# Performance work log

Hardware: AMD Instinct MI355X
Metric: run time of the kernel (lower is better)

The kernel has to match this reference:

```python
import jax, jax.numpy as jnp
import numpy as np

VOCAB = 32000; DIM = 512; NL = 6; B = 2; L = 1024
DI = 2 * DIM      # d_inner (expand=2)
DS = 16           # d_state
DC = 4            # d_conv
DR = DIM // 16    # dt_rank = ceil(512/16) = 32


def setup_inputs() -> dict:
    key = jax.random.key(0)
    ks = jax.random.split(key, 10)
    s = 0.02
    tokens = jax.random.randint(ks[0], (B, L), 0, VOCAB)
    pos_emb = jax.random.normal(ks[1], (1, L, DIM)) * s
    embed = jax.random.normal(ks[2], (VOCAB, DIM)) * s
    lm_w = jax.random.normal(ks[3], (VOCAB, DIM)) * s
    lm_b = jnp.zeros((VOCAB,), jnp.float32)
    in_proj_w = jax.random.normal(ks[4], (NL, 2 * DI, DIM)) * s
    conv_w = jax.random.normal(ks[5], (NL, DI, DC)) * s
    conv_b = jnp.zeros((NL, DI), jnp.float32)
    x_proj_w = jax.random.normal(ks[6], (NL, DR + 2 * DS, DI)) * s
    dt_proj_w = jax.random.normal(ks[7], (NL, DI, DR)) * s
    dt_proj_b = jnp.broadcast_to(jnp.log(jnp.expm1(jnp.float32(0.01))), (NL, DI)).astype(jnp.float32)
    A_log = jnp.log(jnp.broadcast_to(jnp.arange(1, DS + 1, dtype=jnp.float32), (NL, DI, DS)))
    Dp = jnp.ones((NL, DI), jnp.float32)
    out_w = jax.random.normal(ks[8], (NL, DIM, DI)) * s
    ln_g = jnp.ones((NL, DIM), jnp.float32)
    ln_b = jnp.zeros((NL, DIM), jnp.float32)
    return dict(tokens=tokens, pos_emb=pos_emb, embed=embed, lm_w=lm_w, lm_b=lm_b,
                in_proj_w=in_proj_w, conv_w=conv_w, conv_b=conv_b, x_proj_w=x_proj_w,
                dt_proj_w=dt_proj_w, dt_proj_b=dt_proj_b, A_log=A_log, Dp=Dp,
                out_w=out_w, ln_g=ln_g, ln_b=ln_b)


def silu(x):
    return x * jax.nn.sigmoid(x)


def layernorm(x, g, b, eps=1e-5):
    mu = jnp.mean(x, -1, keepdims=True)
    var = jnp.var(x, -1, keepdims=True)
    return (x - mu) * jax.lax.rsqrt(var + eps) * g + b


def causal_dwconv(x, w, b):
    # x: (B,L,DI), w: (DI,DC) depthwise, left-pad causal
    xp = jnp.pad(x, ((0, 0), (DC - 1, 0), (0, 0)))
    y = b
    for k in range(DC):
        y = y + w[:, k] * xp[:, k:k + x.shape[1], :]
    return y


def selective_scan(u, dt, A, Bm, Cm, Dp):
    # u,dt: (B,L,DI); A: (DI,DS); Bm,Cm: (B,L,DS)
    dA = jnp.exp(dt[..., None] * A)                       # (B,L,DI,DS)
    dBu = dt[..., None] * Bm[:, :, None, :] * u[..., None]
    h0 = jnp.zeros((u.shape[0], DI, DS), u.dtype)

    def step(h, inp):
        dA_t, dBu_t, C_t = inp
        h = dA_t * h + dBu_t
        y = jnp.einsum('bdn,bn->bd', h, C_t)
        return h, y

    _, ys = jax.lax.scan(step, h0, (dA.transpose(1, 0, 2, 3),
                                    dBu.transpose(1, 0, 2, 3),
                                    Cm.transpose(1, 0, 2)))
    return ys.transpose(1, 0, 2) + u * Dp


def mamba_block(x, in_w, cw, cb, xp_w, dtw, dtb, A_log, Dp, ow):
    xz = jnp.einsum('bld,ed->ble', x, in_w)               # (B,L,2*DI)
    xc, z = jnp.split(xz, 2, axis=-1)
    xc = silu(causal_dwconv(xc, cw, cb))
    x_dbl = jnp.einsum('bld,ed->ble', xc, xp_w)           # (B,L,DR+2*DS)
    dt, Bm, Cm = jnp.split(x_dbl, [DR, DR + DS], axis=-1)
    dt = jax.nn.softplus(jnp.einsum('blr,dr->bld', dt, dtw) + dtb)
    A = -jnp.exp(A_log)
    y = selective_scan(xc, dt, A, Bm, Cm, Dp)
    y = y * silu(z)
    return jnp.einsum('bld,ed->ble', y, ow)


def reference(tokens, pos_emb, embed, lm_w, lm_b, in_proj_w, conv_w, conv_b,
              x_proj_w, dt_proj_w, dt_proj_b, A_log, Dp, out_w, ln_g, ln_b):
    x = embed[tokens] + pos_emb[:, :tokens.shape[1]]
    for i in range(NL):
        res = x
        x = mamba_block(x, in_proj_w[i], conv_w[i], conv_b[i], x_proj_w[i],
                        dt_proj_w[i], dt_proj_b[i], A_log[i], Dp[i], out_w[i])
        x = layernorm(x + res, ln_g[i], ln_b[i])
    return jnp.einsum('bld,vd->blv', x, lm_w) + lm_b
```

## Files before the change

### kernel.cpp

```cpp
#include <hip/hip_runtime.h>
#include <hip/hip_bf16.h>
#include <math.h>

#define BB 2
#define LL 1024
#define DIM 512
#define NL 6
#define DI 1024
#define DS 16
#define DC 4
#define DR 32
#define VOCAB 32000
#define M_ROWS (BB * LL)
#define CCH 64
#define CHLEN (LL / CCH)
#define KSPLIT 8
#define OSPLIT 2

typedef unsigned short u16;
typedef __attribute__((ext_vector_type(8))) short bf16x8;
typedef __attribute__((ext_vector_type(4))) float f32x4;

__device__ __forceinline__ u16 f2bf(float f) {
    unsigned u = __float_as_uint(f);
    u += 0x7FFF + ((u >> 16) & 1);
    return (u16)(u >> 16);
}
__device__ __forceinline__ float bf2f(u16 h) {
    return __uint_as_float(((unsigned)h) << 16);
}
#define SWZ(r, c) ((c) ^ (((r) >> 1) & 3))

__global__ __launch_bounds__(256) void cast_all(const float* __restrict__ lm,
                                                const float* __restrict__ inw,
                                                const float* __restrict__ ow,
                                                const float* __restrict__ xp,
                                                u16* __restrict__ lmb,
                                                u16* __restrict__ inb,
                                                u16* __restrict__ owb_,
                                                u16* __restrict__ xpb) {
    int idx = blockIdx.x * 256 + threadIdx.x;
    const float* src; u16* dst; int off;
    if (idx < 2048000)      { src = lm;  dst = lmb;  off = idx; }
    else if (idx < 2834432) { src = inw; dst = inb;  off = idx - 2048000; }
    else if (idx < 3227648) { src = ow;  dst = owb_; off = idx - 2834432; }
    else                    { src = xp;  dst = xpb;  off = idx - 3227648; }
    float4 v0 = ((const float4*)src)[off * 2];
    float4 v1 = ((const float4*)src)[off * 2 + 1];
    union { u16 h[8]; int4 v; } r;
    r.h[0] = f2bf(v0.x); r.h[1] = f2bf(v0.y); r.h[2] = f2bf(v0.z); r.h[3] = f2bf(v0.w);
    r.h[4] = f2bf(v1.x); r.h[5] = f2bf(v1.y); r.h[6] = f2bf(v1.z); r.h[7] = f2bf(v1.w);
    ((int4*)dst)[off] = r.v;
}

__global__ __launch_bounds__(256) void embed_kernel(const int* __restrict__ tok,
                                                    const float* __restrict__ pos,
                                                    const float* __restrict__ emb,
                                                    float* __restrict__ x,
                                                    u16* __restrict__ xb) {
    int idx = blockIdx.x * 256 + threadIdx.x;
    int d = idx & (DIM - 1);
    int l = (idx >> 9) & (LL - 1);
    int b = idx >> 19;
    int t = tok[b * LL + l];
    float v = emb[(size_t)t * DIM + d] + pos[l * DIM + d];
    x[idx] = v;
    xb[idx] = f2bf(v);
}

__global__ __launch_bounds__(512) void gemm_256(const u16* __restrict__ A,
                                                const u16* __restrict__ W,
                                                float* __restrict__ C,
                                                const float* __restrict__ bias,
                                                int K, int N) {
    __shared__ __align__(16) char smem_raw[98304];
    u16* As = (u16*)smem_raw;
    u16* Ws = (u16*)(smem_raw + 49152);
    float* Cs = (float*)smem_raw;

    const int t = threadIdx.x;
    const int l = t & 63;
    const int w = t >> 6;
    const int wr = w >> 2;
    const int wc = w & 3;

    const int nwg = gridDim.x;
    const int q8 = nwg >> 3, r8 = nwg & 7;
    const int xcd = blockIdx.x & 7, rank = blockIdx.x >> 3;
    const int wgid = (xcd < r8 ? xcd * (q8 + 1) : r8 * (q8 + 1) + (xcd - r8) * q8) + rank;
    const int bm = (wgid & 7) * 256;
    const int bn = (wgid >> 3) * 256;

    f32x4 acc[8][4] = {};
    const int nt = K >> 5;

    auto STAGE = [&](int bufi, int k0) {
#pragma unroll
        for (int p = 0; p < 2; ++p) {
            const int g = p * 512 + t;
            const int row = g >> 2, slot = g & 3;
            __builtin_amdgcn_global_load_lds(
                (const __attribute__((address_space(1))) unsigned int*)
                    (A + (size_t)(bm + row) * K + k0 + SWZ(row, slot) * 8),
                (__attribute__((address_space(3))) unsigned int*)
                    (As + bufi * 8192 + (p * 512 + w * 64) * 8),
                16, 0, 0);
        }
#pragma unroll
        for (int p = 0; p < 2; ++p) {
            const int g = p * 512 + t;
            const int row = g >> 2, slot = g & 3;
            __builtin_amdgcn_global_load_lds(
                (const __attribute__((address_space(1))) unsigned int*)
                    (W + (size_t)(bn + row) * K + k0 + SWZ(row, slot) * 8),
                (__attribute__((address_space(3))) unsigned int*)
                    (Ws + bufi * 8192 + (p * 512 + w * 64) * 8),
                16, 0, 0);
        }
    };
    auto COMPUTE = [&](int bufi) {
        const u16* Ab = As + bufi * 8192;
        const u16* Wb = Ws + bufi * 8192;
        bf16x8 bfr[4];
#pragma unroll
        for (int ni = 0; ni < 4; ++ni) {
            const int wrow = wc * 64 + ni * 16 + (l & 15);
            bfr[ni] = *(const bf16x8*)(Wb + wrow * 32 + SWZ(wrow, l >> 4) * 8);
        }
#pragma unroll
        for (int mi = 0; mi < 8; ++mi) {
            const int arow = wr * 128 + mi * 16 + (l & 15);
            bf16x8 a = *(const bf16x8*)(Ab + arow * 32 + SWZ(arow, l >> 4) * 8);
#pragma unroll
            for (int ni = 0; ni < 4; ++ni)
                acc[mi][ni] = __builtin_amdgcn_mfma_f32_16x16x32_bf16(bfr[ni], a, acc[mi][ni], 0, 0, 0);
        }
    };

    STAGE(0, 0);
    STAGE(1, 32);
    int b0 = 0;
    for (int tt = 0; tt < nt - 2; ++tt) {
        int b2 = b0 + 2; if (b2 >= 3) b2 -= 3;
        STAGE(b2, (tt + 2) << 5);
        asm volatile("s_waitcnt vmcnt(8)\ns_barrier" ::: "memory");
        COMPUTE(b0);
        asm volatile("s_waitcnt lgkmcnt(0)\ns_barrier" ::: "memory");
        ++b0; if (b0 == 3) b0 = 0;
    }
    asm volatile("s_waitcnt vmcnt(4)\ns_barrier" ::: "memory");
    COMPUTE(b0);
    asm volatile("s_waitcnt lgkmcnt(0)\ns_barrier" ::: "memory");
    ++b0; if (b0 == 3) b0 = 0;
    asm volatile("s_waitcnt vmcnt(0)\ns_barrier" ::: "memory");
    COMPUTE(b0);
    asm volatile("s_waitcnt lgkmcnt(0)" ::: "memory");
    __syncthreads();

#pragma unroll
    for (int pass = 0; pass < 4; ++pass) {
        if (wr == (pass >> 1)) {
            const int pm0 = (pass & 1) * 4;
#pragma unroll
            for (int mi2 = 0; mi2 < 4; ++mi2) {
                const int r = mi2 * 16 + (l & 15);
#pragma unroll
                for (int ni = 0; ni < 4; ++ni) {
                    const int c = wc * 64 + ni * 16 + ((l >> 4) << 2);
                    float4 v;
                    v.x = acc[pm0 + mi2][ni][0]; v.y = acc[pm0 + mi2][ni][1];
                    v.z = acc[pm0 + mi2][ni][2]; v.w = acc[pm0 + mi2][ni][3];
                    *(float4*)(Cs + r * 260 + c) = v;
                }
            }
        }
        __syncthreads();
#pragma unroll
        for (int it = 0; it < 8; ++it) {
            const int idx = it * 512 + t;
            const int r = idx >> 6;
            const int c4 = (idx & 63) * 4;
            float4 v = *(float4*)(Cs + r * 260 + c4);
            if (bias != nullptr) {
                float4 b4 = *(const float4*)(bias + bn + c4);
                v.x += b4.x; v.y += b4.y; v.z += b4.z; v.w += b4.w;
            }
            *(float4*)(C + (size_t)(bm + pass * 64 + r) * N + bn + c4) = v;
        }
        __syncthreads();
    }
}

__global__ __launch_bounds__(256) void gemm_n64(const u16* __restrict__ A,
                                                const u16* __restrict__ W,
                                                float* __restrict__ out,
                                                u16* __restrict__ outb,
                                                const float* __restrict__ bias,
                                                int lda, int ldw, int ldc,
                                                int KS, int pstride) {
    __shared__ __align__(16) char smem_raw[36864];
    u16* As = (u16*)smem_raw;
    u16* Ws = (u16*)(smem_raw + 24576);
    float* Cs = (float*)smem_raw;

    const int t = threadIdx.x;
    const int l = t & 63;
    const int w = t >> 6;
    const int gx = gridDim.x, gy = gridDim.y;
    const int nwg = gx * gy * gridDim.z;
    const int fid = (blockIdx.z * gy + blockIdx.y) * gx + blockIdx.x;
    const int q8 = nwg >> 3, r8 = nwg & 7;
    const int xcd = fid & 7, rank = fid >> 3;
    const int wgid = (xcd < r8 ? xcd * (q8 + 1) : r8 * (q8 + 1) + (xcd - r8) * q8) + rank;
    const int kz = wgid % gx;
    const int bm = ((wgid / gx) % gy) * 128;
    const int bnn = (wgid / (gx * gy)) * 64;
    const int wm = w * 32;

    f32x4 acc[2][4] = {};
    const int nt = KS >> 5;
    const int kbeg = kz * KS;

    auto STAGE = [&](int bufi, int k0) {
#pragma unroll
        for (int p = 0; p < 2; ++p) {
            const int i = p * 256 + w * 64 + l;
            const int row = i >> 2;
            const int kq = SWZ(row, i & 3);
            __builtin_amdgcn_global_load_lds(
                (const __attribute__((address_space(1))) unsigned int*)
                    (A + (size_t)(bm + row) * lda + k0 + kq * 8),
                (__attribute__((address_space(3))) unsigned int*)
                    (As + bufi * 4096 + (p * 256 + w * 64) * 8),
                16, 0, 0);
        }
        {
            const int i = w * 64 + l;
            const int row = i >> 2;
            const int kq = SWZ(row, i & 3);
            __builtin_amdgcn_global_load_lds(
                (const __attribute__((address_space(1))) unsigned int*)
                    (W + (size_t)(bnn + row) * ldw + k0 + kq * 8),
                (__attribute__((address_space(3))) unsigned int*)
                    (Ws + bufi * 2048 + (w * 64) * 8),
                16, 0, 0);
        }
    };
    auto COMPUTE = [&](int bufi) {
        const u16* Ab = As + bufi * 4096;
        const u16* Wb = Ws + bufi * 2048;
        bf16x8 bfr[4];
#pragma unroll
        for (int ni = 0; ni < 4; ++ni) {
            const int wr2 = ni * 16 + (l & 15);
            bfr[ni] = *(const bf16x8*)(Wb + wr2 * 32 + SWZ(wr2, l >> 4) * 8);
        }
#pragma unroll
        for (int mi = 0; mi < 2; ++mi) {
            const int ar = wm + mi * 16 + (l & 15);
            bf16x8 a = *(const bf16x8*)(Ab + ar * 32 + SWZ(ar, l >> 4) * 8);
#pragma unroll
            for (int ni = 0; ni < 4; ++ni)
                acc[mi][ni] = __builtin_amdgcn_mfma_f32_16x16x32_bf16(bfr[ni], a, acc[mi][ni], 0, 0, 0);
        }
    };

    STAGE(0, kbeg);
    if (nt == 1) {
        asm volatile("s_waitcnt vmcnt(0)\ns_barrier" ::: "memory");
        COMPUTE(0);
        asm volatile("s_waitcnt lgkmcnt(0)" ::: "memory");
    } else {
        STAGE(1, kbeg + 32);
        int b0 = 0;
        for (int tt = 0; tt < nt - 2; ++tt) {
            int b2 = b0 + 2; if (b2 >= 3) b2 -= 3;
            STAGE(b2, kbeg + ((tt + 2) << 5));
            asm volatile("s_waitcnt vmcnt(6)\ns_barrier" ::: "memory");
            COMPUTE(b0);
            asm volatile("s_waitcnt lgkmcnt(0)\ns_barrier" ::: "memory");
            ++b0; if (b0 == 3) b0 = 0;
        }
        asm volatile("s_waitcnt vmcnt(3)\ns_barrier" ::: "memory");
        COMPUTE(b0);
        asm volatile("s_waitcnt lgkmcnt(0)\ns_barrier" ::: "memory");
        ++b0; if (b0 == 3) b0 = 0;
        asm volatile("s_waitcnt vmcnt(0)\ns_barrier" ::: "memory");
        COMPUTE(b0);
        asm volatile("s_waitcnt lgkmcnt(0)" ::: "memory");
    }

    if (outb != nullptr) {
        u16* opb = outb + (size_t)kz * pstride;
#pragma unroll
        for (int mi = 0; mi < 2; ++mi) {
            const int row = bm + wm + mi * 16 + (l & 15);
#pragma unroll
            for (int ni = 0; ni < 4; ++ni) {
                const int col = bnn + ni * 16 + ((l >> 4) << 2);
                ushort4 v;
                v.x = f2bf(acc[mi][ni][0]); v.y = f2bf(acc[mi][ni][1]);
                v.z = f2bf(acc[mi][ni][2]); v.w = f2bf(acc[mi][ni][3]);
                *(ushort4*)(opb + (size_t)row * ldc + col) = v;
            }
        }
    } else {
        float* op = out + (size_t)kz * pstride;
        __syncthreads();
#pragma unroll
        for (int pass = 0; pass < 2; ++pass) {
            if ((w >> 1) == pass) {
                const int rbase = (w & 1) * 32;
#pragma unroll
                for (int mi = 0; mi < 2; ++mi) {
                    const int r = rbase + mi * 16 + (l & 15);
#pragma unroll
                    for (int ni = 0; ni < 4; ++ni) {
                        const int c = ni * 16 + ((l >> 4) << 2);
                        float4 v;
                        v.x = acc[mi][ni][0]; v.y = acc[mi][ni][1];
                        v.z = acc[mi][ni][2]; v.w = acc[mi][ni][3];
                        *(float4*)(Cs + r * 65 + c) = v;
                    }
                }
            }
            __syncthreads();
#pragma unroll
            for (int it = 0; it < 4; ++it) {
                const int idx = it * 256 + t;
                const int r = idx >> 4;
                const int c4 = (idx & 15) * 4;
                float4 v = *(float4*)(Cs + r * 65 + c4);
                if (bias != nullptr) {
                    float4 b4 = *(const float4*)(bias + bnn + c4);
                    v.x += b4.x; v.y += b4.y; v.z += b4.z; v.w += b4.w;
                }
                *(float4*)(op + (size_t)(bm + pass * 64 + r) * ldc + bnn + c4) = v;
            }
            __syncthreads();
        }
    }
}

__global__ __launch_bounds__(256) void conv_silu(const u16* __restrict__ xzb,
                                                 const float* __restrict__ cw,
                                                 const float* __restrict__ cb,
                                                 u16* __restrict__ xcb) {
    int idx8 = blockIdx.x * 256 + threadIdx.x;
    int c0 = (idx8 & 127) * 8;
    int m = idx8 >> 7;
    int l = m & (LL - 1);

    float acc[8];
    float4 cb0 = *(const float4*)(cb + c0);
    float4 cb1 = *(const float4*)(cb + c0 + 4);
    acc[0] = cb0.x; acc[1] = cb0.y; acc[2] = cb0.z; acc[3] = cb0.w;
    acc[4] = cb1.x; acc[5] = cb1.y; acc[6] = cb1.z; acc[7] = cb1.w;
#pragma unroll
    for (int k = 0; k < DC; ++k) {
        int ll = l + k - (DC - 1);
        if (ll < 0) continue;
        const u16* row = xzb + ((size_t)(m + k - (DC - 1))) * (2 * DI) + c0;
        ushort4 r0 = *(const ushort4*)row;
        ushort4 r1 = *(const ushort4*)(row + 4);
#pragma unroll
        for (int j = 0; j < 4; ++j) {
            acc[j]     += cw[(c0 + j) * DC + k]     * bf2f(((const u16*)&r0)[j]);
            acc[j + 4] += cw[(c0 + j + 4) * DC + k] * bf2f(((const u16*)&r1)[j]);
        }
    }
    ushort4 o0, o1;
#pragma unroll
    for (int j = 0; j < 4; ++j) {
        float v0 = acc[j]     / (1.f + __expf(-acc[j]));
        float v1 = acc[j + 4] / (1.f + __expf(-acc[j + 4]));
        ((u16*)&o0)[j] = f2bf(v0);
        ((u16*)&o1)[j] = f2bf(v1);
    }
    u16* op = xcb + (size_t)idx8 * 8;
    *(ushort4*)op = o0;
    *(ushort4*)(op + 4) = o1;
}

__global__ __launch_bounds__(256) void scan_pass1(const u16* __restrict__ xcb,
                                                  const float* __restrict__ Pf,
                                                  const float* __restrict__ dtw,
                                                  const float* __restrict__ dtb,
                                                  const float* __restrict__ A_log,
                                                  float* __restrict__ S,
                                                  float* __restrict__ Q) {
    __shared__ float xds[CHLEN][64];
    const int t = threadIdx.x;
    const int d = blockIdx.x * 256 + t;
    const int b = blockIdx.y;
    const int c = blockIdx.z;
    const int l0 = c * CHLEN;
    const int m0 = b * LL + l0;

    for (int i = t; i < CHLEN * 64; i += 256) {
        int r = i >> 6, cc = i & 63;
        float s = 0.f;
#pragma unroll
        for (int kz = 0; kz < KSPLIT; ++kz)
            s += Pf[(size_t)kz * (M_ROWS * 64) + (m0 + r) * 64 + cc];
        xds[r][cc] = s;
    }
    __syncthreads();

    float4 wreg[8];
#pragma unroll
    for (int kk = 0; kk < 8; ++kk)
        wreg[kk] = *(const float4*)(dtw + (size_t)d * DR + kk * 4);
    const float dtbv = dtb[d];

    float a[DS];
#pragma unroll
    for (int q = 0; q < 4; ++q) {
        float4 al = *(const float4*)(A_log + d * DS + q * 4);
        a[q * 4 + 0] = -__expf(al.x);
        a[q * 4 + 1] = -__expf(al.y);
        a[q * 4 + 2] = -__expf(al.z);
        a[q * 4 + 3] = -__expf(al.w);
    }
    float Qr[DS];
#pragma unroll
    for (int n = 0; n < DS; ++n) Qr[n] = 0.f;
    float Ssum = 0.f;

    const u16* up = xcb + (size_t)m0 * DI + d;

    for (int l = 0; l < CHLEN; ++l) {
        float dacc = dtbv;
#pragma unroll
        for (int kk = 0; kk < 8; ++kk) {
            float4 xv = *(const float4*)&xds[l][kk * 4];
            dacc += wreg[kk].x * xv.x + wreg[kk].y * xv.y +
                    wreg[kk].z * xv.z + wreg[kk].w * xv.w;
        }
        float dtv = (dacc > 20.f) ? dacc : log1pf(__expf(dacc));
        float uv = bf2f(up[(size_t)l * DI]);
        float wv = dtv * uv;
        Ssum += dtv;
#pragma unroll
        for (int q = 0; q < 4; ++q) {
            float4 Bv = *(const float4*)&xds[l][32 + q * 4];
            float dA0 = __expf(dtv * a[q * 4 + 0]);
            float dA1 = __expf(dtv * a[q * 4 + 1]);
            float dA2 = __expf(dtv * a[q * 4 + 2]);
            float dA3 = __expf(dtv * a[q * 4 + 3]);
            Qr[q * 4 + 0] = dA0 * Qr[q * 4 + 0] + wv * Bv.x;
            Qr[q * 4 + 1] = dA1 * Qr[q * 4 + 1] + wv * Bv.y;
            Qr[q * 4 + 2] = dA2 * Qr[q * 4 + 2] + wv * Bv.z;
            Qr[q * 4 + 3] = dA3 * Qr[q * 4 + 3] + wv * Bv.w;
        }
    }
    S[((size_t)b * CCH + c) * DI + d] = Ssum;
    float* Qp = Q + (((size_t)b * CCH + c) * DI + d) * DS;
#pragma unroll
    for (int q = 0; q < 4; ++q) {
        float4 o;
        o.x = Qr[q * 4 + 0]; o.y = Qr[q * 4 + 1];
        o.z = Qr[q * 4 + 2]; o.w = Qr[q * 4 + 3];
        *(float4*)(Qp + q * 4) = o;
    }
}

__global__ __launch_bounds__(64) void scan_pass2(const float* __restrict__ A_log,
                                                 const float* __restrict__ S,
                                                 float* __restrict__ Q) {
    const int idx = blockIdx.x * 64 + threadIdx.x;
    const int b = idx >> 14;
    const int dn = idx & 16383;
    const int d = dn >> 4;
    const float a = -__expf(A_log[dn]);
    float h = 0.f;
    for (int c = 0; c < CCH; ++c) {
        const size_t soff = ((size_t)b * CCH + c) * DI + d;
        const size_t qoff = ((size_t)b * CCH + c) * (size_t)(DI * DS) + dn;
        float P = __expf(a * S[soff]);
        float qv = Q[qoff];
        Q[qoff] = h;
        h = P * h + qv;
    }
}

__global__ __launch_bounds__(256) void scan_pass3(const u16* __restrict__ xcb,
                                                  const float* __restrict__ Pf,
                                                  const float* __restrict__ dtw,
                                                  const float* __restrict__ dtb,
                                                  const u16* __restrict__ xzb,
                                                  const float* __restrict__ A_log,
                                                  const float* __restrict__ Dpp,
                                                  const float* __restrict__ Q,
                                                  u16* __restrict__ y) {
    __shared__ float xds[CHLEN][64];
    const int t = threadIdx.x;
    const int d = blockIdx.x * 256 + t;
    const int b = blockIdx.y;
    const int c = blockIdx.z;
    const int l0 = c * CHLEN;
    const int m0 = b * LL + l0;

    for (int i = t; i < CHLEN * 64; i += 256) {
        int r = i >> 6, cc = i & 63;
        float s = 0.f;
#pragma unroll
        for (int kz = 0; kz < KSPLIT; ++kz)
            s += Pf[(size_t)kz * (M_ROWS * 64) + (m0 + r) * 64 + cc];
        xds[r][cc] = s;
    }
    __syncthreads();

    float4 wreg[8];
#pragma unroll
    for (int kk = 0; kk < 8; ++kk)
        wreg[kk] = *(const float4*)(dtw + (size_t)d * DR + kk * 4);
    const float dtbv = dtb[d];

    float a[DS];
#pragma unroll
    for (int q = 0; q < 4; ++q) {
        float4 al = *(const float4*)(A_log + d * DS + q * 4);
        a[q * 4 + 0] = -__expf(al.x);
        a[q * 4 + 1] = -__expf(al.y);
        a[q * 4 + 2] = -__expf(al.z);
        a[q * 4 + 3] = -__expf(al.w);
    }
    float h[DS];
    const float* Qp = Q + (((size_t)b * CCH + c) * DI + d) * DS;
#pragma unroll
    for (int q = 0; q < 4; ++q) {
        float4 hv = *(const float4*)(Qp + q * 4);
        h[q * 4 + 0] = hv.x; h[q * 4 + 1] = hv.y;
        h[q * 4 + 2] = hv.z; h[q * 4 + 3] = hv.w;
    }
    const float dp = Dpp[d];

    const u16* up = xcb + (size_t)m0 * DI + d;
    const u16* zp = xzb + (size_t)m0 * (2 * DI) + DI + d;
    u16* yp = y + (size_t)m0 * DI + d;

    for (int l = 0; l < CHLEN; ++l) {
        float dacc = dtbv;
#pragma unroll
        for (int kk = 0; kk < 8; ++kk) {
            float4 xv = *(const float4*)&xds[l][kk * 4];
            dacc += wreg[kk].x * xv.x + wreg[kk].y * xv.y +
                    wreg[kk].z * xv.z + wreg[kk].w * xv.w;
        }
        float dtv = (dacc > 20.f) ? dacc : log1pf(__expf(dacc));
        float uv = bf2f(up[(size_t)l * DI]);
        float wv = dtv * uv;
        float p = 0.f;
#pragma unroll
        for (int q = 0; q < 4; ++q) {
            float4 Bv = *(const float4*)&xds[l][32 + q * 4];
            float4 Cv = *(const float4*)&xds[l][48 + q * 4];
            float dA0 = __expf(dtv * a[q * 4 + 0]);
            float dA1 = __expf(dtv * a[q * 4 + 1]);
            float dA2 = __expf(dtv * a[q * 4 + 2]);
            float dA3 = __expf(dtv * a[q * 4 + 3]);
            h[q * 4 + 0] = dA0 * h[q * 4 + 0] + wv * Bv.x;
            h[q * 4 + 1] = dA1 * h[q * 4 + 1] + wv * Bv.y;
            h[q * 4 + 2] = dA2 * h[q * 4 + 2] + wv * Bv.z;
            h[q * 4 + 3] = dA3 * h[q * 4 + 3] + wv * Bv.w;
            p += h[q * 4 + 0] * Cv.x + h[q * 4 + 1] * Cv.y +
                 h[q * 4 + 2] * Cv.z + h[q * 4 + 3] * Cv.w;
        }
        float zv = bf2f(zp[(size_t)l * (2 * DI)]);
        float g = zv / (1.f + __expf(-zv));
        yp[(size_t)l * DI] = f2bf((p + uv * dp) * g);
    }
}

__global__ __launch_bounds__(256) void add_ln(const float* __restrict__ opart,
                                              float* __restrict__ x,
                                              const float* __restrict__ g,
                                              const float* __restrict__ b,
                                              u16* __restrict__ xb) {
    const int PS = M_ROWS * DIM;
    int m = blockIdx.x;
    int t = threadIdx.x;
    const float* xr = x + (size_t)m * DIM;
    float v0 = xr[t];
    float v1 = xr[t + 256];
#pragma unroll
    for (int kz = 0; kz < OSPLIT; ++kz) {
        const float* op = opart + (size_t)kz * PS + (size_t)m * DIM;
        v0 += op[t];
        v1 += op[t + 256];
    }
    float s = v0 + v1;
    float ss = v0 * v0 + v1 * v1;
#pragma unroll
    for (int off = 32; off > 0; off >>= 1) {
        s += __shfl_down(s, off, 64);
        ss += __shfl_down(ss, off, 64);
    }
    __shared__ float sb[4], ssb[4];
    int w = t >> 6;
    if ((t & 63) == 0) { sb[w] = s; ssb[w] = ss; }
    __syncthreads();
    float stot = sb[0] + sb[1] + sb[2] + sb[3];
    float sstot = ssb[0] + ssb[1] + ssb[2] + ssb[3];
    float mean = stot * (1.f / DIM);
    float var = sstot * (1.f / DIM) - mean * mean;
    float rs = rsqrtf(var + 1e-5f);
    float* xw = x + (size_t)m * DIM;
    float o0 = (v0 - mean) * rs * g[t] + b[t];
    float o1 = (v1 - mean) * rs * g[t + 256] + b[t + 256];
    xw[t] = o0;
    xw[t + 256] = o1;
    xb[(size_t)m * DIM + t] = f2bf(o0);
    xb[(size_t)m * DIM + t + 256] = f2bf(o1);
}

extern "C" void kernel_launch(void* const* d_in, const int* in_sizes, int n_in,
                              void* d_out, int out_size, void* d_ws, size_t ws_size,
                              hipStream_t stream) {
    const int*   tokens = (const int*)d_in[0];
    const float* pos    = (const float*)d_in[1];
    const float* emb    = (const float*)d_in[2];
    const float* lm_w   = (const float*)d_in[3];
    const float* lm_b   = (const float*)d_in[4];
    const float* in_w   = (const float*)d_in[5];
    const float* cw     = (const float*)d_in[6];
    const float* cb     = (const float*)d_in[7];
    const float* xpw    = (const float*)d_in[8];
    const float* dtw    = (const float*)d_in[9];
    const float* dtb    = (const float*)d_in[10];
    const float* A_log  = (const float*)d_in[11];
    const float* Dpp    = (const float*)d_in[12];
    const float* ow     = (const float*)d_in[13];
    const float* lng    = (const float*)d_in[14];
    const float* lnb    = (const float*)d_in[15];
    float* out = (float*)d_out;

    float* ws = (float*)d_ws;
    float* x    = ws;
    float* S    = x + 1048576;
    float* Qb   = S + 131072;
    float* Pf   = Qb + 2097152;
    float* Pf2  = Pf + 1048576;
    u16* xzb    = (u16*)(Pf2 + 2097152);
    u16* xb     = xzb + 4194304;
    u16* yb     = xb + 1048576;
    u16* xcb    = yb + 2097152;
    u16* lm_wb  = xcb + 2097152;
    u16* in_wb  = lm_wb + 16384000;
    u16* owb    = in_wb + 6291456;
    u16* xpwb   = owb + 3145728;

    cast_all<<<12800, 256, 0, stream>>>(lm_w, in_w, ow, xpw,
                                        lm_wb, in_wb, owb, xpwb);

    embed_kernel<<<M_ROWS * DIM / 256, 256, 0, stream>>>(tokens, pos, emb, x, xb);

    for (int i = 0; i < NL; ++i) {
        gemm_n64<<<dim3(1, M_ROWS / 128, 2048 / 64), 256, 0, stream>>>(
            xb, in_wb + (size_t)i * 2048 * 512, nullptr, xzb, nullptr,
            512, 512, 2048, 512, 0);
        conv_silu<<<M_ROWS * DI / 8 / 256, 256, 0, stream>>>(
            xzb, cw + (size_t)i * DI * DC, cb + (size_t)i * DI, xcb);
        gemm_n64<<<dim3(KSPLIT, M_ROWS / 128, 1), 256, 0, stream>>>(
            xcb, xpwb + (size_t)i * 64 * 1024, Pf, nullptr, nullptr,
            1024, 1024, 64, 1024 / KSPLIT, M_ROWS * 64);
        scan_pass1<<<dim3(DI / 256, BB, CCH), 256, 0, stream>>>(
            xcb, Pf, dtw + (size_t)i * DI * DR, dtb + (size_t)i * DI,
            A_log + (size_t)i * DI * DS, S, Qb);
        scan_pass2<<<(BB * DI * DS) / 64, 64, 0, stream>>>(
            A_log + (size_t)i * DI * DS, S, Qb);
        scan_pass3<<<dim3(DI / 256, BB, CCH), 256, 0, stream>>>(
            xcb, Pf, dtw + (size_t)i * DI * DR, dtb + (size_t)i * DI, xzb,
            A_log + (size_t)i * DI * DS, Dpp + (size_t)i * DI, Qb, yb);
        gemm_n64<<<dim3(OSPLIT, M_ROWS / 128, 512 / 64), 256, 0, stream>>>(
            yb, owb + (size_t)i * 512 * 1024, Pf2, nullptr, nullptr,
            1024, 1024, 512, 1024 / OSPLIT, M_ROWS * 512);
        add_ln<<<M_ROWS, 256, 0, stream>>>(
            Pf2, x, lng + (size_t)i * DIM, lnb + (size_t)i * DIM, xb);
    }

    gemm_256<<<(M_ROWS / 256) * (VOCAB / 256), 512, 0, stream>>>(
        xb, lm_wb, out, lm_b, 512, VOCAB);
}
```

Measured before the change: 794.5 us.

## Switch gemm_256 to double buffering with direct register epilogue and MFMA priority

The large GEMM goes from a 3-stage to a 2-stage LDS pipeline, shrinking shared memory from 96KB to 64KB. Its LDS-staged epilogue is replaced by direct float4 stores from accumulators, and s_setprio raises wave priority around the MFMA loops in both GEMM kernels. The aim is to cut LDS footprint and epilogue barriers, possibly allowing more occupancy. In exchange it loses one stage of load latency hiding and writes output in a less coalesced pattern (4 floats per lane per row).

```diff
diff --git a/kernel.cpp b/kernel.cpp
--- a/kernel.cpp
+++ b/kernel.cpp
@@ -73,10 +73,8 @@
                                                 float* __restrict__ C,
                                                 const float* __restrict__ bias,
                                                 int K, int N) {
-    __shared__ __align__(16) char smem_raw[98304];
-    u16* As = (u16*)smem_raw;
-    u16* Ws = (u16*)(smem_raw + 49152);
-    float* Cs = (float*)smem_raw;
+    __shared__ __align__(16) u16 As[2 * 8192];
+    __shared__ __align__(16) u16 Ws[2 * 8192];
 
     const int t = threadIdx.x;
     const int l = t & 63;
@@ -127,6 +125,7 @@
             const int wrow = wc * 64 + ni * 16 + (l & 15);
             bfr[ni] = *(const bf16x8*)(Wb + wrow * 32 + SWZ(wrow, l >> 4) * 8);
         }
+        __builtin_amdgcn_s_setprio(1);
 #pragma unroll
         for (int mi = 0; mi < 8; ++mi) {
             const int arow = wr * 128 + mi * 16 + (l & 15);
@@ -135,59 +134,36 @@
             for (int ni = 0; ni < 4; ++ni)
                 acc[mi][ni] = __builtin_amdgcn_mfma_f32_16x16x32_bf16(bfr[ni], a, acc[mi][ni], 0, 0, 0);
         }
+        __builtin_amdgcn_s_setprio(0);
     };
 
     STAGE(0, 0);
-    STAGE(1, 32);
-    int b0 = 0;
-    for (int tt = 0; tt < nt - 2; ++tt) {
-        int b2 = b0 + 2; if (b2 >= 3) b2 -= 3;
-        STAGE(b2, (tt + 2) << 5);
-        asm volatile("s_waitcnt vmcnt(8)\ns_barrier" ::: "memory");
-        COMPUTE(b0);
+    for (int tt = 0; tt < nt; ++tt) {
+        if (tt + 1 < nt) {
+            STAGE((tt + 1) & 1, (tt + 1) << 5);
+            asm volatile("s_waitcnt vmcnt(4)\ns_barrier" ::: "memory");
+        } else {
+            asm volatile("s_waitcnt vmcnt(0)\ns_barrier" ::: "memory");
+        }
+        COMPUTE(tt & 1);
         asm volatile("s_waitcnt lgkmcnt(0)\ns_barrier" ::: "memory");
-        ++b0; if (b0 == 3) b0 = 0;
-    }
-    asm volatile("s_waitcnt vmcnt(4)\ns_barrier" ::: "memory");
-    COMPUTE(b0);
-    asm volatile("s_waitcnt lgkmcnt(0)\ns_barrier" ::: "memory");
-    ++b0; if (b0 == 3) b0 = 0;
-    asm volatile("s_waitcnt vmcnt(0)\ns_barrier" ::: "memory");
-    COMPUTE(b0);
-    asm volatile("s_waitcnt lgkmcnt(0)" ::: "memory");
-    __syncthreads();
-
-#pragma unroll
-    for (int pass = 0; pass < 4; ++pass) {
-        if (wr == (pass >> 1)) {
-            const int pm0 = (pass & 1) * 4;
-#pragma unroll
-            for (int mi2 = 0; mi2 < 4; ++mi2) {
-                const int r = mi2 * 16 + (l & 15);
-#pragma unroll
-                for (int ni = 0; ni < 4; ++ni) {
-                    const int c = wc * 64 + ni * 16 + ((l >> 4) << 2);
-                    float4 v;
-                    v.x = acc[pm0 + mi2][ni][0]; v.y = acc[pm0 + mi2][ni][1];
-                    v.z = acc[pm0 + mi2][ni][2]; v.w = acc[pm0 + mi2][ni][3];
-                    *(float4*)(Cs + r * 260 + c) = v;
-                }
-            }
-        }
-        __syncthreads();
-#pragma unroll
-        for (int it = 0; it < 8; ++it) {
-            const int idx = it * 512 + t;
-            const int r = idx >> 6;
-            const int c4 = (idx & 63) * 4;
-            float4 v = *(float4*)(Cs + r * 260 + c4);
+    }
+
+#pragma unroll
+    for (int mi = 0; mi < 8; ++mi) {
+        const int row = bm + wr * 128 + mi * 16 + (l & 15);
+#pragma unroll
+        for (int ni = 0; ni < 4; ++ni) {
+            const int col = bn + wc * 64 + ni * 16 + ((l >> 4) << 2);
+            float4 v;
+            v.x = acc[mi][ni][0]; v.y = acc[mi][ni][1];
+            v.z = acc[mi][ni][2]; v.w = acc[mi][ni][3];
             if (bias != nullptr) {
-                float4 b4 = *(const float4*)(bias + bn + c4);
+                float4 b4 = *(const float4*)(bias + col);
                 v.x += b4.x; v.y += b4.y; v.z += b4.z; v.w += b4.w;
             }
-            *(float4*)(C + (size_t)(bm + pass * 64 + r) * N + bn + c4) = v;
-        }
-        __syncthreads();
+            *(float4*)(C + (size_t)row * N + col) = v;
+        }
     }
 }
 
@@ -255,6 +231,7 @@
             const int wr2 = ni * 16 + (l & 15);
             bfr[ni] = *(const bf16x8*)(Wb + wr2 * 32 + SWZ(wr2, l >> 4) * 8);
         }
+        __builtin_amdgcn_s_setprio(1);
 #pragma unroll
         for (int mi = 0; mi < 2; ++mi) {
             const int ar = wm + mi * 16 + (l & 15);
@@ -263,6 +240,7 @@
             for (int ni = 0; ni < 4; ++ni)
                 acc[mi][ni] = __builtin_amdgcn_mfma_f32_16x16x32_bf16(bfr[ni], a, acc[mi][ni], 0, 0, 0);
         }
+        __builtin_amdgcn_s_setprio(0);
     };
 
     STAGE(0, kbeg);
```

New measurement: 818.1 us. 3.0% more time.
